# Performance work log

Measured on AMD Instinct MI355X. Metric: run time of the kernel, lower is better.

## Reference

```python
import jax, jax.numpy as jnp
import numpy as np

H = 512  # hidden_size


def setup_inputs() -> dict:
    key = jax.random.key(0)
    ks = jax.random.split(key, 13)
    B, S, E, V = 64, 2048, 512, 32000
    s = 0.05
    return {
        "word_input": jax.random.randint(ks[0], (B,), 0, V),
        "last_hidden": jax.random.normal(ks[1], (1, B, H), jnp.float32),
        "encoder_outputs": jax.random.normal(ks[2], (S, B, H), jnp.float32),
        "emb": jax.random.normal(ks[3], (V, E), jnp.float32) * s,
        "attn_W": jax.random.normal(ks[4], (H, 2 * H), jnp.float32) * s,
        "attn_b": jax.random.normal(ks[5], (H,), jnp.float32) * s,
        "v": jax.random.normal(ks[6], (H,), jnp.float32) * s,
        "W_ih": jax.random.normal(ks[7], (3 * H, H + E), jnp.float32) * s,
        "W_hh": jax.random.normal(ks[8], (3 * H, H), jnp.float32) * s,
        "b_ih": jax.random.normal(ks[9], (3 * H,), jnp.float32) * s,
        "b_hh": jax.random.normal(ks[10], (3 * H,), jnp.float32) * s,
        "out_W": jax.random.normal(ks[11], (V, 2 * H), jnp.float32) * s,
        "out_b": jax.random.normal(ks[12], (V,), jnp.float32) * s,
    }


def reference(word_input, last_hidden, encoder_outputs, emb, attn_W, attn_b, v,
              W_ih, W_hh, b_ih, b_hh, out_W, out_b):
    # word_input: [B] int; last_hidden: [1,B,H]; encoder_outputs: [S,B,H]
    hid = last_hidden[-1]                       # [B,H]
    enc = jnp.transpose(encoder_outputs, (1, 0, 2))  # [B,S,H]

    # Bahdanau 'concat' attention: tanh(W [h;e] + b) . v  (split W to avoid [B,S,2H])
    Wa, We = attn_W[:, :H], attn_W[:, H:]
    energy = jnp.tanh((hid @ Wa.T)[:, None, :] + jnp.einsum('bsh,kh->bsk', enc, We) + attn_b)
    scores = jnp.einsum('bsk,k->bs', energy, v)       # [B,S]
    attn = jax.nn.softmax(scores, axis=1)             # [B,S]
    context = jnp.einsum('bs,bsh->bh', attn, enc)     # [B,H]

    # GRU step (PyTorch gate layout: r, z, n)
    x = jnp.concatenate([emb[word_input], context], axis=1)  # [B,E+H]
    gi = x @ W_ih.T + b_ih
    gh = hid @ W_hh.T + b_hh
    r = jax.nn.sigmoid(gi[:, :H] + gh[:, :H])
    z = jax.nn.sigmoid(gi[:, H:2 * H] + gh[:, H:2 * H])
    n = jnp.tanh(gi[:, 2 * H:] + r * gh[:, 2 * H:])
    h_new = (1.0 - z) * n + z * hid                   # [B,H]

    logits = jnp.concatenate([h_new, context], axis=1) @ out_W.T + out_b
    output = jax.nn.log_softmax(logits, axis=1)       # [B,V]
    return output, h_new[None]                        # hidden: [1,B,H]
```

## Files before the change

### kernel.cpp

```cpp
#include <hip/hip_runtime.h>
#include <hip/hip_bf16.h>
#include <cstdint>
#include <cstddef>

#define HD 512
#define BB 64
#define SS 2048
#define VV 32000
#define MM (SS*BB)
#define NCH 32

typedef __attribute__((ext_vector_type(8))) short bf16x8;
typedef __attribute__((ext_vector_type(4))) float f32x4;

static __device__ __forceinline__ unsigned pack2(float a, float b) {
    unsigned r;
    asm("v_cvt_pk_bf16_f32 %0, %1, %2" : "=v"(r) : "v"(a), "v"(b));
    return r;
}
static __device__ __forceinline__ float rcp_fast(float x) {
    float r; asm("v_rcp_f32 %0, %1" : "=v"(r) : "v"(x)); return r;
}
static __device__ __forceinline__ float tanh_fast(float x) {
    float e = __expf(2.f * x);
    return 1.f - 2.f * rcp_fast(e + 1.f);
}
static __device__ __forceinline__ float sigmoid_fast(float x) {
    return 1.f / (1.f + __expf(-x));
}
static __device__ __forceinline__ void gload16(const void* g, void* l) {
    __builtin_amdgcn_global_load_lds(
        (const __attribute__((address_space(1))) void*)g,
        (__attribute__((address_space(3))) void*)l, 16, 0, 0);
}

#define WAITL   asm volatile("s_waitcnt lgkmcnt(0)" ::: "memory")
#define WAITVL(N) asm volatile("s_waitcnt vmcnt(" #N ") lgkmcnt(0)" ::: "memory")
#define SBAR    __builtin_amdgcn_s_barrier()
#define SCHED   __builtin_amdgcn_sched_barrier(0)

__global__ void prep_kernel(const float* __restrict__ hid,
                            const float* __restrict__ attn_W,
                            const float* __restrict__ attn_b,
                            float* __restrict__ qc,
                            uint4* __restrict__ WeB4) {
    int i = blockIdx.x * 256 + threadIdx.x;
    int n = i >> 6, b = i & 63;
    const float* hrow = hid + b * HD;
    const float* wrow = attn_W + (size_t)n * (2 * HD);
    float acc = 0.f;
    for (int k = 0; k < HD; k += 4) {
        float4 h4 = *(const float4*)(hrow + k);
        float4 w4 = *(const float4*)(wrow + k);
        acc += h4.x * w4.x + h4.y * w4.y + h4.z * w4.z + h4.w * w4.w;
    }
    qc[b * HD + n] = acc + attn_b[n];
    int col = (i << 3) & 511;
    int cc0 = col >> 3;
    const float* src = attn_W + (size_t)n * (2 * HD) + HD + col;
    float4 f0 = *(const float4*)(src);
    float4 f1 = *(const float4*)(src + 4);
    uint4 p;
    p.x = pack2(f0.x, f0.y); p.y = pack2(f0.z, f0.w);
    p.z = pack2(f1.x, f1.y); p.w = pack2(f1.z, f1.w);
    int ccs = (cc0 & ~7) | ((cc0 & 7) ^ (n & 7));
    WeB4[n * 64 + ccs] = p;
}

__global__ __launch_bounds__(512, 2) void fattn_kernel(
    const float* __restrict__ enc,
    const uint4* __restrict__ WeB4,
    const float* __restrict__ qc,
    const float* __restrict__ vvec,
    float* __restrict__ oP,
    float* __restrict__ lP)
{
    __shared__ char smem[8192 + 65536 + 2048 + 256];
    uint4* Ald = (uint4*)smem;
    uint4* Bld = (uint4*)(smem + 8192);
    float (*red)[8] = (float(*)[8])(smem + 8192 + 65536);
    float* p_lds = (float*)(smem + 8192 + 65536 + 2048);
    float* opart = (float*)(smem + 8192);

    const int tid = threadIdx.x;
    const int wv = tid >> 6, lane = tid & 63, l15 = lane & 15, l4 = lane >> 4;
    const int b = blockIdx.x & 63;
    const int c = blockIdx.x >> 6;
    const int s0 = c * 64;

    f32x4 acc[4][4] = {};

    const int arow = tid >> 3;
    const int ac8 = tid & 7;
    const float* aptr = enc + ((size_t)(s0 + arow) * 64 + b) * HD + ac8 * 8;
    const int aslot = arow * 8 + (ac8 ^ (arow & 7));

    const int brow = wv * 8 + (lane >> 3);
    const uint4* bg = WeB4 + (size_t)brow * 64 + (lane & 7);

    for (int t = 0; t < 8; ++t) {
        __syncthreads();
        float4 a0 = *(const float4*)(aptr + t * 64);
        float4 a1 = *(const float4*)(aptr + t * 64 + 4);
#pragma unroll
        for (int i = 0; i < 8; ++i)
            gload16(bg + (size_t)i * 64 * 64 + t * 8, &Bld[i * 512 + tid]);
        uint4 u;
        u.x = pack2(a0.x, a0.y); u.y = pack2(a0.z, a0.w);
        u.z = pack2(a1.x, a1.y); u.w = pack2(a1.z, a1.w);
        Ald[aslot] = u;
        __syncthreads();

#pragma unroll
        for (int ks = 0; ks < 2; ++ks) {
            const int chunk = ks * 4 + l4;
            bf16x8 af[4], bfr[4];
#pragma unroll
            for (int mi = 0; mi < 4; ++mi) {
                int row = mi * 16 + l15;
                af[mi] = *(const bf16x8*)&Ald[row * 8 + (chunk ^ (row & 7))];
            }
#pragma unroll
            for (int ni = 0; ni < 4; ++ni) {
                int row = wv * 64 + ni * 16 + l15;
                bfr[ni] = *(const bf16x8*)&Bld[row * 8 + (chunk ^ (row & 7))];
            }
#pragma unroll
            for (int mi = 0; mi < 4; ++mi)
#pragma unroll
                for (int ni = 0; ni < 4; ++ni)
                    acc[mi][ni] = __builtin_amdgcn_mfma_f32_16x16x32_bf16(
                        af[mi], bfr[ni], acc[mi][ni], 0, 0, 0);
        }
    }

    float vv[4], qn[4];
#pragma unroll
    for (int ni = 0; ni < 4; ++ni) {
        int n = wv * 64 + ni * 16 + l15;
        vv[ni] = vvec[n];
        qn[ni] = qc[b * HD + n];
    }
#pragma unroll
    for (int mi = 0; mi < 4; ++mi) {
#pragma unroll
        for (int r = 0; r < 4; ++r) {
            const int rowl = mi * 16 + l4 * 4 + r;
            float s = 0.f;
#pragma unroll
            for (int ni = 0; ni < 4; ++ni)
                s += tanh_fast(acc[mi][ni][r] + qn[ni]) * vv[ni];
#pragma unroll
            for (int msk = 8; msk >= 1; msk >>= 1)
                s += __shfl_xor(s, msk);
            if (l15 == 0) red[rowl][wv] = s;
        }
    }
    __syncthreads();
    if (tid < 64) {
        float t = ((red[tid][0] + red[tid][1]) + (red[tid][2] + red[tid][3]))
                + ((red[tid][4] + red[tid][5]) + (red[tid][6] + red[tid][7]));
        float p = __expf(t);
        p_lds[tid] = p;
        float l = p;
#pragma unroll
        for (int msk = 32; msk >= 1; msk >>= 1) l += __shfl_xor(l, msk);
        if (tid == 0) lP[b * NCH + c] = l;
    }
    __syncthreads();

    float o8[8] = {};
    const float* ebase = enc + ((size_t)(s0 + wv * 8) * 64 + b) * HD + lane * 8;
#pragma unroll
    for (int i = 0; i < 8; ++i) {
        float w = p_lds[wv * 8 + i];
        const float* ep = ebase + (size_t)i * 64 * HD;
        float4 e0 = *(const float4*)(ep);
        float4 e1 = *(const float4*)(ep + 4);
        o8[0] += w * e0.x; o8[1] += w * e0.y; o8[2] += w * e0.z; o8[3] += w * e0.w;
        o8[4] += w * e1.x; o8[5] += w * e1.y; o8[6] += w * e1.z; o8[7] += w * e1.w;
    }
    {
        float4* dst = (float4*)&opart[wv * 512 + lane * 8];
        float4 w0 = {o8[0], o8[1], o8[2], o8[3]};
        float4 w1 = {o8[4], o8[5], o8[6], o8[7]};
        dst[0] = w0; dst[1] = w1;
    }
    __syncthreads();
    float o = 0.f;
#pragma unroll
    for (int w = 0; w < 8; ++w) o += opart[w * 512 + tid];
    oP[((size_t)b * NCH + c) * HD + tid] = o;
}

__global__ void combine_kernel(const float* __restrict__ oP,
                               const float* __restrict__ lP,
                               const int* __restrict__ word,
                               const float* __restrict__ emb,
                               float* __restrict__ x,
                               unsigned* __restrict__ y_bf) {
    const int b = blockIdx.x;
    const int tid = threadIdx.x;
    __shared__ float ctx_lds[512];
    float L = 0.f;
#pragma unroll 8
    for (int c = 0; c < NCH; ++c) L += lP[b * NCH + c];
    float o = 0.f;
#pragma unroll 4
    for (int c = 0; c < NCH; ++c)
        o += oP[((size_t)b * NCH + c) * HD + tid];
    float ctx = o / L;
    x[b * 1024 + HD + tid] = ctx;
    ctx_lds[tid] = ctx;
    x[b * 1024 + tid] = emb[(size_t)word[b] * HD + tid];
    __syncthreads();
    if (tid < 256)
        y_bf[b * 512 + 256 + tid] = pack2(ctx_lds[2 * tid], ctx_lds[2 * tid + 1]);
}

__global__ void gates_kernel(const float* __restrict__ x,
                             const float* __restrict__ hid,
                             const float* __restrict__ W_ih,
                             const float* __restrict__ W_hh,
                             const float* __restrict__ b_ih,
                             const float* __restrict__ b_hh,
                             float* __restrict__ gi, float* __restrict__ gh) {
    const int tid = threadIdx.x;
    const int b = tid & 63;
    const int j = blockIdx.x * 4 + (tid >> 6);
    float agi = 0.f, agh = 0.f;
    const float* xr = x + b * 1024;
    const float* wr = W_ih + (size_t)j * 1024;
    for (int k = 0; k < 1024; k += 4) {
        float4 xv = *(const float4*)(xr + k);
        float4 w4 = *(const float4*)(wr + k);
        agi += xv.x * w4.x + xv.y * w4.y + xv.z * w4.z + xv.w * w4.w;
    }
    const float* hr = hid + b * HD;
    const float* wh = W_hh + (size_t)j * HD;
    for (int k = 0; k < HD; k += 4) {
        float4 hv = *(const float4*)(hr + k);
        float4 w4 = *(const float4*)(wh + k);
        agh += hv.x * w4.x + hv.y * w4.y + hv.z * w4.z + hv.w * w4.w;
    }
    gi[b * 1536 + j] = agi + b_ih[j];
    gh[b * 1536 + j] = agh + b_hh[j];
}

__global__ void hnew_kernel(const float* __restrict__ gi,
                            const float* __restrict__ gh,
                            const float* __restrict__ hid,
                            float* __restrict__ out_h,
                            unsigned* __restrict__ y_bf) {
    const int b = blockIdx.x;
    const int h = threadIdx.x * 2;
    float hn[2];
#pragma unroll
    for (int j = 0; j < 2; ++j) {
        int hh = h + j;
        float r = sigmoid_fast(gi[b * 1536 + hh] + gh[b * 1536 + hh]);
        float z = sigmoid_fast(gi[b * 1536 + 512 + hh] + gh[b * 1536 + 512 + hh]);
        float n = tanh_fast(gi[b * 1536 + 1024 + hh] + r * gh[b * 1536 + 1024 + hh]);
        hn[j] = (1.f - z) * n + z * hid[b * HD + hh];
        out_h[b * HD + hh] = hn[j];
    }
    y_bf[b * 512 + (h >> 1)] = pack2(hn[0], hn[1]);
}

__global__ __launch_bounds__(256, 4) void logits_kernel(
    const unsigned short* __restrict__ y_bf,
    const float* __restrict__ out_W,
    const float* __restrict__ out_b,
    float* __restrict__ logits)
{
    __shared__ uint4 Yld[64 * 8];
    __shared__ uint4 Wld[64 * 8];
    const int tid = threadIdx.x;
    const int wv = tid >> 6, lane = tid & 63, l15 = lane & 15, l4 = lane >> 4;
    const int n0 = blockIdx.x * 64;

    f32x4 acc[4] = {};

    const int s1 = tid, s2 = tid + 256;
    const int r1 = s1 >> 3, g1 = (s1 & 7) ^ (r1 & 7);
    const int r2 = s2 >> 3, g2 = (s2 & 7) ^ (r2 & 7);
    const unsigned short* ya1 = y_bf + (size_t)r1 * 1024 + g1 * 8;
    const unsigned short* ya2 = y_bf + (size_t)r2 * 1024 + g2 * 8;

    const int wr = tid >> 3, wc8 = tid & 7;
    const int wsl = wc8 ^ (wr & 7);
    const float* wp0 = out_W + (size_t)(n0 + wr) * 1024 + wc8 * 8;
    const float* wp1 = out_W + (size_t)(n0 + wr + 32) * 1024 + wc8 * 8;

    float4 pw[2][4];
    pw[0][0] = *(const float4*)(wp0);
    pw[0][1] = *(const float4*)(wp0 + 4);
    pw[0][2] = *(const float4*)(wp1);
    pw[0][3] = *(const float4*)(wp1 + 4);

#pragma unroll
    for (int t = 0; t < 16; ++t) {
        const int cur = t & 1;
        if (t > 0) {
            WAITL; SBAR; SCHED;
        }
        gload16(ya1 + t * 64, &Yld[s1]);
        gload16(ya2 + t * 64, &Yld[s2]);
        {
            uint4 u;
            u.x = pack2(pw[cur][0].x, pw[cur][0].y);
            u.y = pack2(pw[cur][0].z, pw[cur][0].w);
            u.z = pack2(pw[cur][1].x, pw[cur][1].y);
            u.w = pack2(pw[cur][1].z, pw[cur][1].w);
            Wld[wr * 8 + wsl] = u;
            u.x = pack2(pw[cur][2].x, pw[cur][2].y);
            u.y = pack2(pw[cur][2].z, pw[cur][2].w);
            u.z = pack2(pw[cur][3].x, pw[cur][3].y);
            u.w = pack2(pw[cur][3].z, pw[cur][3].w);
            Wld[(wr + 32) * 8 + wsl] = u;
        }
        if (t < 15) {
            const int k1 = (t + 1) * 64;
            pw[cur ^ 1][0] = *(const float4*)(wp0 + k1);
            pw[cur ^ 1][1] = *(const float4*)(wp0 + k1 + 4);
            pw[cur ^ 1][2] = *(const float4*)(wp1 + k1);
            pw[cur ^ 1][3] = *(const float4*)(wp1 + k1 + 4);
            WAITVL(4);
        } else {
            WAITVL(0);
        }
        SBAR; SCHED;

#pragma unroll
        for (int ks = 0; ks < 2; ++ks) {
            const int chunk = ks * 4 + l4;
            bf16x8 af[4], bfr;
#pragma unroll
            for (int mi = 0; mi < 4; ++mi) {
                int row = mi * 16 + l15;
                af[mi] = *(const bf16x8*)&Yld[row * 8 + (chunk ^ (row & 7))];
            }
            {
                int row = wv * 16 + l15;
                bfr = *(const bf16x8*)&Wld[row * 8 + (chunk ^ (row & 7))];
            }
#pragma unroll
            for (int mi = 0; mi < 4; ++mi)
                acc[mi] = __builtin_amdgcn_mfma_f32_16x16x32_bf16(
                    af[mi], bfr, acc[mi], 0, 0, 0);
        }
    }
#pragma unroll
    for (int mi = 0; mi < 4; ++mi) {
#pragma unroll
        for (int r = 0; r < 4; ++r) {
            const int b = mi * 16 + l4 * 4 + r;
            int n = n0 + wv * 16 + l15;
            logits[(size_t)b * VV + n] = acc[mi][r] + out_b[n];
        }
    }
}

__global__ void lsm1_kernel(const float* __restrict__ logits,
                            float* __restrict__ part) {
    const int bid = blockIdx.x;
    const int b = bid / 5, q = bid - b * 5;
    const int tid = threadIdx.x;
    __shared__ float sm[256];
    const float* row = logits + (size_t)b * VV + q * 6400;
    float m = -1e30f;
    for (int i = tid; i < 6400; i += 256) m = fmaxf(m, row[i]);
    sm[tid] = m; __syncthreads();
    for (int o = 128; o > 0; o >>= 1) {
        if (tid < o) sm[tid] = fmaxf(sm[tid], sm[tid + o]);
        __syncthreads();
    }
    m = sm[0]; __syncthreads();
    float s = 0.f;
    for (int i = tid; i < 6400; i += 256) s += __expf(row[i] - m);
    sm[tid] = s; __syncthreads();
    for (int o = 128; o > 0; o >>= 1) {
        if (tid < o) sm[tid] += sm[tid + o];
        __syncthreads();
    }
    if (tid == 0) { part[bid * 2] = m; part[bid * 2 + 1] = sm[0]; }
}

__global__ void lsm2_kernel(float* __restrict__ logits,
                            const float* __restrict__ part) {
    const int bid = blockIdx.x;
    const int b = bid / 5, q = bid - b * 5;
    const int tid = threadIdx.x;
    float m = -1e30f;
#pragma unroll
    for (int c = 0; c < 5; ++c) m = fmaxf(m, part[(b * 5 + c) * 2]);
    float L = 0.f;
#pragma unroll
    for (int c = 0; c < 5; ++c)
        L += part[(b * 5 + c) * 2 + 1] * __expf(part[(b * 5 + c) * 2] - m);
    float lse = m + __logf(L);
    float* row = logits + (size_t)b * VV + q * 6400;
    for (int i = tid; i < 6400; i += 256) row[i] -= lse;
}

extern "C" void kernel_launch(void* const* d_in, const int* in_sizes, int n_in,
                              void* d_out, int out_size, void* d_ws, size_t ws_size,
                              hipStream_t stream) {
    (void)in_sizes; (void)n_in; (void)out_size; (void)ws_size;
    const int*   word   = (const int*)d_in[0];
    const float* hid    = (const float*)d_in[1];
    const float* enc    = (const float*)d_in[2];
    const float* emb    = (const float*)d_in[3];
    const float* attn_W = (const float*)d_in[4];
    const float* attn_b = (const float*)d_in[5];
    const float* v      = (const float*)d_in[6];
    const float* W_ih   = (const float*)d_in[7];
    const float* W_hh   = (const float*)d_in[8];
    const float* b_ih   = (const float*)d_in[9];
    const float* b_hh   = (const float*)d_in[10];
    const float* out_W  = (const float*)d_in[11];
    const float* out_b  = (const float*)d_in[12];

    float* out    = (float*)d_out;
    float* logits = out;
    float* out_h  = out + (size_t)BB * VV;

    char* ws0 = (char*)d_ws;
    size_t off = 0;
    float* qc      = (float*)(ws0 + off);    off += 64 * 512 * 4;
    uint4* WeB4    = (uint4*)(ws0 + off);    off += 512 * 512 * 2;
    float* oP      = (float*)(ws0 + off);    off += (size_t)BB * NCH * HD * 4;
    float* lP      = (float*)(ws0 + off);    off += BB * NCH * 4;
    float* x       = (float*)(ws0 + off);    off += 64 * 1024 * 4;
    unsigned* y_bf = (unsigned*)(ws0 + off); off += 64 * 1024 * 2;
    float* gi      = (float*)(ws0 + off);    off += 64 * 1536 * 4;
    float* gh      = (float*)(ws0 + off);    off += 64 * 1536 * 4;
    float* lsmp    = (float*)(ws0 + off);    off += 320 * 2 * 4;

    prep_kernel<<<128, 256, 0, stream>>>(hid, attn_W, attn_b, qc, WeB4);
    fattn_kernel<<<BB * NCH, 512, 0, stream>>>(enc, WeB4, qc, v, oP, lP);
    combine_kernel<<<BB, 512, 0, stream>>>(oP, lP, word, emb, x, y_bf);
    gates_kernel<<<384, 256, 0, stream>>>(x, hid, W_ih, W_hh, b_ih, b_hh, gi, gh);
    hnew_kernel<<<BB, 256, 0, stream>>>(gi, gh, hid, out_h, y_bf);
    logits_kernel<<<VV / 64, 256, 0, stream>>>((const unsigned short*)y_bf, out_W, out_b, logits);
    lsm1_kernel<<<320, 256, 0, stream>>>(logits, lsmp);
    lsm2_kernel<<<320, 256, 0, stream>>>(logits, lsmp);
}
```

Measured before the change: 328.4 us.

## Process 128 sequence rows per attention block to halve We tile reloads

Each attention block now covers 128 sequence positions instead of 64, which halves the chunk count. Each staged bf16 We tile in LDS is reused across twice as many MFMA row tiles, and there are half as many partial outputs for the combine kernel to sum. The reduction scratch now aliases the A tile region, so an extra barrier was added, and the per-block sum is reduced across two waves. The accumulator array doubles to 128 floats per lane under launch_bounds(512,2), which risks register pressure or spilling, and the grid shrinks to 1024 blocks.

Result: slower. 354.0 us (+7.8%).

```diff
diff --git a/kernel.cpp b/kernel.cpp
--- a/kernel.cpp
+++ b/kernel.cpp
@@ -8,7 +8,7 @@
 #define SS 2048
 #define VV 32000
 #define MM (SS*BB)
-#define NCH 32
+#define NCH 16
 
 typedef __attribute__((ext_vector_type(8))) short bf16x8;
 typedef __attribute__((ext_vector_type(4))) float f32x4;
@@ -75,48 +75,55 @@
     float* __restrict__ oP,
     float* __restrict__ lP)
 {
-    __shared__ char smem[8192 + 65536 + 2048 + 256];
+    __shared__ char smem[16384 + 65536];
     uint4* Ald = (uint4*)smem;
-    uint4* Bld = (uint4*)(smem + 8192);
-    float (*red)[8] = (float(*)[8])(smem + 8192 + 65536);
-    float* p_lds = (float*)(smem + 8192 + 65536 + 2048);
-    float* opart = (float*)(smem + 8192);
+    uint4* Bld = (uint4*)(smem + 16384);
+    float (*red)[8] = (float(*)[8])smem;
+    float* p_lds = (float*)(smem + 4096);
+    float* opart = (float*)(smem + 16384);
 
     const int tid = threadIdx.x;
     const int wv = tid >> 6, lane = tid & 63, l15 = lane & 15, l4 = lane >> 4;
     const int b = blockIdx.x & 63;
     const int c = blockIdx.x >> 6;
-    const int s0 = c * 64;
-
-    f32x4 acc[4][4] = {};
+    const int s0 = c * 128;
+
+    f32x4 acc[8][4] = {};
 
     const int arow = tid >> 3;
     const int ac8 = tid & 7;
-    const float* aptr = enc + ((size_t)(s0 + arow) * 64 + b) * HD + ac8 * 8;
-    const int aslot = arow * 8 + (ac8 ^ (arow & 7));
+    const float* ap0 = enc + ((size_t)(s0 + arow) * 64 + b) * HD + ac8 * 8;
+    const float* ap1 = enc + ((size_t)(s0 + 64 + arow) * 64 + b) * HD + ac8 * 8;
+    const int asl0 = arow * 8 + (ac8 ^ (arow & 7));
+    const int asl1 = (64 + arow) * 8 + (ac8 ^ (arow & 7));
 
     const int brow = wv * 8 + (lane >> 3);
     const uint4* bg = WeB4 + (size_t)brow * 64 + (lane & 7);
 
     for (int t = 0; t < 8; ++t) {
         __syncthreads();
-        float4 a0 = *(const float4*)(aptr + t * 64);
-        float4 a1 = *(const float4*)(aptr + t * 64 + 4);
+        float4 a0 = *(const float4*)(ap0 + t * 64);
+        float4 a1 = *(const float4*)(ap0 + t * 64 + 4);
+        float4 a2 = *(const float4*)(ap1 + t * 64);
+        float4 a3 = *(const float4*)(ap1 + t * 64 + 4);
 #pragma unroll
         for (int i = 0; i < 8; ++i)
-            gload16(bg + (size_t)i * 64 * 64 + t * 8, &Bld[i * 512 + tid]);
-        uint4 u;
-        u.x = pack2(a0.x, a0.y); u.y = pack2(a0.z, a0.w);
-        u.z = pack2(a1.x, a1.y); u.w = pack2(a1.z, a1.w);
-        Ald[aslot] = u;
+            gload16(bg + (size_t)i * 4096 + t * 8, &Bld[i * 512 + tid]);
+        uint4 u0, u1;
+        u0.x = pack2(a0.x, a0.y); u0.y = pack2(a0.z, a0.w);
+        u0.z = pack2(a1.x, a1.y); u0.w = pack2(a1.z, a1.w);
+        u1.x = pack2(a2.x, a2.y); u1.y = pack2(a2.z, a2.w);
+        u1.z = pack2(a3.x, a3.y); u1.w = pack2(a3.z, a3.w);
+        Ald[asl0] = u0;
+        Ald[asl1] = u1;
         __syncthreads();
 
 #pragma unroll
         for (int ks = 0; ks < 2; ++ks) {
             const int chunk = ks * 4 + l4;
-            bf16x8 af[4], bfr[4];
-#pragma unroll
-            for (int mi = 0; mi < 4; ++mi) {
+            bf16x8 af[8], bfr[4];
+#pragma unroll
+            for (int mi = 0; mi < 8; ++mi) {
                 int row = mi * 16 + l15;
                 af[mi] = *(const bf16x8*)&Ald[row * 8 + (chunk ^ (row & 7))];
             }
@@ -126,7 +133,7 @@
                 bfr[ni] = *(const bf16x8*)&Bld[row * 8 + (chunk ^ (row & 7))];
             }
 #pragma unroll
-            for (int mi = 0; mi < 4; ++mi)
+            for (int mi = 0; mi < 8; ++mi)
 #pragma unroll
                 for (int ni = 0; ni < 4; ++ni)
                     acc[mi][ni] = __builtin_amdgcn_mfma_f32_16x16x32_bf16(
@@ -141,8 +148,9 @@
         vv[ni] = vvec[n];
         qn[ni] = qc[b * HD + n];
     }
-#pragma unroll
-    for (int mi = 0; mi < 4; ++mi) {
+    __syncthreads();
+#pragma unroll
+    for (int mi = 0; mi < 8; ++mi) {
 #pragma unroll
         for (int r = 0; r < 4; ++r) {
             const int rowl = mi * 16 + l4 * 4 + r;
@@ -157,7 +165,7 @@
         }
     }
     __syncthreads();
-    if (tid < 64) {
+    if (tid < 128) {
         float t = ((red[tid][0] + red[tid][1]) + (red[tid][2] + red[tid][3]))
                 + ((red[tid][4] + red[tid][5]) + (red[tid][6] + red[tid][7]));
         float p = __expf(t);
@@ -165,15 +173,16 @@
         float l = p;
 #pragma unroll
         for (int msk = 32; msk >= 1; msk >>= 1) l += __shfl_xor(l, msk);
-        if (tid == 0) lP[b * NCH + c] = l;
+        if (lane == 0) red[0][wv] = l;
     }
     __syncthreads();
+    if (tid == 0) lP[b * NCH + c] = red[0][0] + red[0][1];
 
     float o8[8] = {};
-    const float* ebase = enc + ((size_t)(s0 + wv * 8) * 64 + b) * HD + lane * 8;
-#pragma unroll
-    for (int i = 0; i < 8; ++i) {
-        float w = p_lds[wv * 8 + i];
+    const float* ebase = enc + ((size_t)(s0 + wv * 16) * 64 + b) * HD + lane * 8;
+#pragma unroll
+    for (int i = 0; i < 16; ++i) {
+        float w = p_lds[wv * 16 + i];
         const float* ep = ebase + (size_t)i * 64 * HD;
         float4 e0 = *(const float4*)(ep);
         float4 e1 = *(const float4*)(ep + 4);
@@ -203,7 +212,7 @@
     const int tid = threadIdx.x;
     __shared__ float ctx_lds[512];
     float L = 0.f;
-#pragma unroll 8
+#pragma unroll
     for (int c = 0; c < NCH; ++c) L += lP[b * NCH + c];
     float o = 0.f;
 #pragma unroll 4
```
